# Kernel optimization log

Hardware: AMD Instinct MI355X
Metric: run time of the kernel (lower is better)

The kernel has to match this reference:

```python
import jax, jax.numpy as jnp
import numpy as np

H = 1024          # hidden_dim
N_AVAIL = 32768   # number of available ops (rows of the score matrix)
N_M = 64          # machines
N_OP = 40000      # unfinished ops
N_JOB = 2000      # jobs
L = 4             # policy_num_layers


def setup_inputs() -> dict:
    key = jax.random.key(0)
    ks = jax.random.split(key, 12)
    s_in = (2.0 / (2 * H + 2)) ** 0.5   # kaiming-ish scale
    s_h = (2.0 / H) ** 0.5
    return {
        "x_m": jax.random.normal(ks[0], (N_M, H), jnp.float32),
        "x_op": jax.random.normal(ks[1], (N_OP, H), jnp.float32),
        "job_srpt": jax.random.uniform(ks[2], (N_JOB,), jnp.float32),
        "pt": jax.random.uniform(ks[3], (N_AVAIL,), jnp.float32),  # process_time / max_process_time
        "W0": jax.random.normal(ks[4], (2 * H + 2, H), jnp.float32) * s_in,
        "b0": jnp.zeros((H,), jnp.float32),
        "W1": jax.random.normal(ks[5], (H, H), jnp.float32) * s_h,
        "b1": jnp.zeros((H,), jnp.float32),
        "W2": jax.random.normal(ks[6], (H, H), jnp.float32) * s_h,
        "b2": jnp.zeros((H,), jnp.float32),
        "W3": jax.random.normal(ks[7], (H, 1), jnp.float32) * s_h,
        "b3": jnp.zeros((1,), jnp.float32),
        "m_ids": jax.random.randint(ks[8], (N_AVAIL,), 0, N_M, jnp.int32),
        "op_idx": jax.random.randint(ks[9], (N_AVAIL,), 0, N_OP, jnp.int32),
        "job_ids": jax.random.randint(ks[10], (N_AVAIL,), 0, N_JOB, jnp.int32),
    }


def reference(x_m, x_op, job_srpt, pt, W0, b0, W1, b1, W2, b2, W3, b3,
              m_ids, op_idx, job_ids):
    # Batched gather + concat: replaces the per-op Python loop of torch.cat's.
    feat = jnp.concatenate(
        [x_m[m_ids],                     # [N, H]
         x_op[op_idx],                   # [N, H]
         job_srpt[job_ids][:, None],     # [N, 1]
         pt[:, None]],                   # [N, 1]
        axis=1)                          # [N, 2H+2]
    lrelu = lambda v: jax.nn.leaky_relu(v, 0.01)
    h = lrelu(feat @ W0 + b0)
    h = lrelu(h @ W1 + b1)
    h = lrelu(h @ W2 + b2)
    score = (h @ W3 + b3).ravel()        # [N]
    probs = jax.nn.softmax(score)        # softmax over available ops (dim=0)
    idx = jnp.argmax(score)              # greedy action
    return probs, idx
```

## Files before the change

kernel.cpp:

```cpp
#include <hip/hip_runtime.h>
#include <hip/hip_bf16.h>

typedef __attribute__((ext_vector_type(8))) short short8;
typedef __attribute__((ext_vector_type(4))) float f32x4;

#define GL2LDS16(g, l)                                                         \
  __builtin_amdgcn_global_load_lds(                                            \
      (const __attribute__((address_space(1))) unsigned int*)(g),              \
      (__attribute__((address_space(3))) unsigned int*)(l), 16, 0, 0)

__global__ __launch_bounds__(256) void feat_kernel(
    const float* __restrict__ x_m, const float* __restrict__ x_op,
    const float* __restrict__ job_srpt, const int* __restrict__ m_ids,
    const int* __restrict__ op_idx, const int* __restrict__ job_ids,
    __hip_bfloat16* __restrict__ feat, float* __restrict__ srow) {
  const int row = blockIdx.x;
  const int t = threadIdx.x;
  const int j0 = t * 8;
  const float* src;
  if (j0 < 1024)
    src = x_m + (long)m_ids[row] * 1024 + j0;
  else
    src = x_op + (long)op_idx[row] * 1024 + (j0 - 1024);
  float4 v0 = *(const float4*)src;
  float4 v1 = *(const float4*)(src + 4);
  union {
    __hip_bfloat16 h[8];
    int4 i4;
  } u;
  u.h[0] = __float2bfloat16(v0.x);
  u.h[1] = __float2bfloat16(v0.y);
  u.h[2] = __float2bfloat16(v0.z);
  u.h[3] = __float2bfloat16(v0.w);
  u.h[4] = __float2bfloat16(v1.x);
  u.h[5] = __float2bfloat16(v1.y);
  u.h[6] = __float2bfloat16(v1.z);
  u.h[7] = __float2bfloat16(v1.w);
  *(int4*)&feat[(long)row * 2048 + j0] = u.i4;
  if (t == 0) srow[row] = job_srpt[job_ids[row]];
}

__global__ __launch_bounds__(256) void wconv_kernel(
    const float* __restrict__ W, __hip_bfloat16* __restrict__ Wt, int K) {
  __shared__ float tile[64][65];
  const int kb = blockIdx.x * 64;
  const int nb = blockIdx.y * 64;
  const int t = threadIdx.x;
#pragma unroll
  for (int it = 0; it < 16; ++it) {
    int idx = it * 256 + t;
    int kk = idx >> 6, nn = idx & 63;
    tile[kk][nn] = W[(long)(kb + kk) * 1024 + nb + nn];
  }
  __syncthreads();
#pragma unroll
  for (int it = 0; it < 16; ++it) {
    int idx = it * 256 + t;
    int nn = idx >> 6, kk = idx & 63;
    Wt[(long)(nb + nn) * K + kb + kk] = __float2bfloat16(tile[kk][nn]);
  }
}

__global__ __launch_bounds__(512, 2) void gemm_kernel(
    const __hip_bfloat16* __restrict__ A, const __hip_bfloat16* __restrict__ Bt,
    __hip_bfloat16* __restrict__ C, const float* __restrict__ bias, int M,
    int N, int K, int rank2, const float* __restrict__ wr0,
    const float* __restrict__ wr1, const float* __restrict__ srow,
    const float* __restrict__ ptv, int fuseW3,
    const float* __restrict__ W3, float* __restrict__ scoreOut) {
  __shared__ __align__(16) __hip_bfloat16 As[2][256 * 64];
  __shared__ __align__(16) __hip_bfloat16 Bs[2][256 * 64];
  const int t = threadIdx.x;
  const int lane = t & 63;
  const int wid = t >> 6;
  const int wm = wid >> 2;
  const int wn = wid & 3;
  const long arow0 = (long)blockIdx.x * 256;
  const int bcol0 = blockIdx.y * 256;
  const int NT = K >> 6;

  f32x4 acc[8][4] = {};

  auto stage = [&](int buf, int kt) {
#pragma unroll
    for (int it = 0; it < 4; ++it) {
      int cc = it * 512 + t;
      int r = cc >> 3, c8 = (cc & 7) ^ (r & 7);
      GL2LDS16(A + (arow0 + r) * (long)K + kt * 64 + c8 * 8, &As[buf][cc * 8]);
    }
#pragma unroll
    for (int it = 0; it < 4; ++it) {
      int cc = it * 512 + t;
      int r = cc >> 3, c8 = (cc & 7) ^ (r & 7);
      GL2LDS16(Bt + (long)(bcol0 + r) * (long)K + kt * 64 + c8 * 8,
               &Bs[buf][cc * 8]);
    }
  };

  stage(0, 0);

  for (int kt = 0; kt < NT; ++kt) {
    const int cur = kt & 1;
    if (kt + 1 < NT) {
      stage(cur ^ 1, kt + 1);
      asm volatile("s_waitcnt vmcnt(8)" ::: "memory");
    } else {
      asm volatile("s_waitcnt vmcnt(0)" ::: "memory");
    }
    __builtin_amdgcn_s_barrier();
    asm volatile("" ::: "memory");

#pragma unroll
    for (int ks = 0; ks < 2; ++ks) {
      const int ko = (ks * 32 + ((lane >> 4) << 3)) ^ ((lane & 7) << 3);
      short8 af[8], bfr[4];
#pragma unroll
      for (int i = 0; i < 8; ++i)
        af[i] =
            *(const short8*)&As[cur][(wm * 128 + i * 16 + (lane & 15)) * 64 + ko];
#pragma unroll
      for (int j = 0; j < 4; ++j)
        bfr[j] =
            *(const short8*)&Bs[cur][(wn * 64 + j * 16 + (lane & 15)) * 64 + ko];
#pragma unroll
      for (int i = 0; i < 8; ++i)
#pragma unroll
        for (int j = 0; j < 4; ++j)
          acc[i][j] = __builtin_amdgcn_mfma_f32_16x16x32_bf16(af[i], bfr[j],
                                                              acc[i][j], 0, 0, 0);
    }

    asm volatile("s_waitcnt lgkmcnt(0)" ::: "memory");
    __builtin_amdgcn_s_barrier();
    asm volatile("" ::: "memory");
  }

  if (!fuseW3) {
#pragma unroll
    for (int j = 0; j < 4; ++j) {
      const int c = bcol0 + wn * 64 + j * 16 + (lane & 15);
      const float bia = bias[c];
      float wa = 0.f, wb = 0.f;
      if (rank2) {
        wa = wr0[c];
        wb = wr1[c];
      }
#pragma unroll
      for (int i = 0; i < 8; ++i) {
        const long rb = arow0 + wm * 128 + i * 16 + ((lane >> 4) << 2);
#pragma unroll
        for (int g = 0; g < 4; ++g) {
          const long r = rb + g;
          float v = acc[i][j][g] + bia;
          if (rank2) v += srow[r] * wa + ptv[r] * wb;
          v = v > 0.f ? v : 0.01f * v;
          C[r * N + c] = __float2bfloat16(v);
        }
      }
    }
  } else {
    float bia[4], w3v[4];
#pragma unroll
    for (int j = 0; j < 4; ++j) {
      const int c = bcol0 + wn * 64 + j * 16 + (lane & 15);
      bia[j] = bias[c];
      w3v[j] = W3[c];
    }
#pragma unroll
    for (int i = 0; i < 8; ++i) {
#pragma unroll
      for (int g = 0; g < 4; ++g) {
        float ps = 0.f;
#pragma unroll
        for (int j = 0; j < 4; ++j) {
          float v = acc[i][j][g] + bia[j];
          v = v > 0.f ? v : 0.01f * v;
          ps += v * w3v[j];
        }
        ps += __shfl_xor(ps, 1);
        ps += __shfl_xor(ps, 2);
        ps += __shfl_xor(ps, 4);
        ps += __shfl_xor(ps, 8);
        if ((lane & 15) == 0) {
          const long r = arow0 + wm * 128 + i * 16 + ((lane >> 4) << 2) + g;
          atomicAdd(&scoreOut[r], ps);
        }
      }
    }
  }
}

__global__ __launch_bounds__(256) void redmax_kernel(
    const float* __restrict__ score, float* __restrict__ pmax,
    int* __restrict__ pidx) {
  const int t = threadIdx.x, b = blockIdx.x;
  float m = -1e30f;
  int mi = 0;
#pragma unroll
  for (int u = 0; u < 2; ++u) {
    int i = b * 512 + u * 256 + t;
    float v = score[i];
    if (v > m) {
      m = v;
      mi = i;
    }
  }
  __shared__ float sm[4];
  __shared__ int si[4];
#pragma unroll
  for (int off = 32; off; off >>= 1) {
    float om = __shfl_down(m, off);
    int oi = __shfl_down(mi, off);
    if (om > m || (om == m && oi < mi)) {
      m = om;
      mi = oi;
    }
  }
  const int lane = t & 63, w = t >> 6;
  if (lane == 0) {
    sm[w] = m;
    si[w] = mi;
  }
  __syncthreads();
  if (t == 0) {
    for (int w2 = 1; w2 < 4; ++w2)
      if (sm[w2] > m || (sm[w2] == m && si[w2] < mi)) {
        m = sm[w2];
        mi = si[w2];
      }
    pmax[b] = m;
    pidx[b] = mi;
  }
}

__global__ __launch_bounds__(64) void finmax_kernel(
    const float* __restrict__ pmax, const int* __restrict__ pidx,
    float* __restrict__ gscal, float* __restrict__ out_idx) {
  const int t = threadIdx.x;
  float m = pmax[t];
  int mi = pidx[t];
#pragma unroll
  for (int off = 32; off; off >>= 1) {
    float om = __shfl_down(m, off);
    int oi = __shfl_down(mi, off);
    if (om > m || (om == m && oi < mi)) {
      m = om;
      mi = oi;
    }
  }
  if (t == 0) {
    gscal[0] = m;
    out_idx[0] = (float)mi;
  }
}

__global__ __launch_bounds__(256) void expsum_kernel(
    const float* __restrict__ score, const float* __restrict__ gscal,
    float* __restrict__ e, float* __restrict__ psum) {
  const int t = threadIdx.x, b = blockIdx.x;
  const float gmax = gscal[0];
  float s = 0.f;
#pragma unroll
  for (int u = 0; u < 2; ++u) {
    int i = b * 512 + u * 256 + t;
    float v = expf(score[i] - gmax);
    e[i] = v;
    s += v;
  }
#pragma unroll
  for (int off = 32; off; off >>= 1) s += __shfl_down(s, off);
  __shared__ float sm[4];
  const int lane = t & 63, w = t >> 6;
  if (lane == 0) sm[w] = s;
  __syncthreads();
  if (t == 0) psum[b] = sm[0] + sm[1] + sm[2] + sm[3];
}

__global__ __launch_bounds__(64) void finsum_kernel(const float* __restrict__ psum,
                                                    float* __restrict__ gscal) {
  float s = psum[threadIdx.x];
#pragma unroll
  for (int off = 32; off; off >>= 1) s += __shfl_down(s, off);
  if (threadIdx.x == 0) gscal[1] = 1.0f / s;
}

__global__ __launch_bounds__(256) void scale_kernel(float* __restrict__ e,
                                                    const float* __restrict__ gscal) {
  const float inv = gscal[1];
  const int i = blockIdx.x * 512 + threadIdx.x;
  e[i] *= inv;
  e[i + 256] *= inv;
}

extern "C" void kernel_launch(void* const* d_in, const int* in_sizes, int n_in,
                              void* d_out, int out_size, void* d_ws,
                              size_t ws_size, hipStream_t stream) {
  const float* x_m = (const float*)d_in[0];
  const float* x_op = (const float*)d_in[1];
  const float* job_srpt = (const float*)d_in[2];
  const float* pt = (const float*)d_in[3];
  const float* W0 = (const float*)d_in[4];
  const float* b0 = (const float*)d_in[5];
  const float* W1 = (const float*)d_in[6];
  const float* b1 = (const float*)d_in[7];
  const float* W2 = (const float*)d_in[8];
  const float* b2 = (const float*)d_in[9];
  const float* W3 = (const float*)d_in[10];
  const int* m_ids = (const int*)d_in[12];
  const int* op_idx = (const int*)d_in[13];
  const int* job_ids = (const int*)d_in[14];

  const int M = 32768;

  char* p = (char*)d_ws;
  __hip_bfloat16* feat = (__hip_bfloat16*)p;            p += (size_t)M * 2048 * 2;
  __hip_bfloat16* hA = (__hip_bfloat16*)p;              p += (size_t)M * 1024 * 2;
  __hip_bfloat16* hB = (__hip_bfloat16*)p;              p += (size_t)M * 1024 * 2;
  __hip_bfloat16* Wt0 = (__hip_bfloat16*)p;             p += (size_t)1024 * 2048 * 2;
  __hip_bfloat16* Wt1 = (__hip_bfloat16*)p;             p += (size_t)1024 * 1024 * 2;
  __hip_bfloat16* Wt2 = (__hip_bfloat16*)p;             p += (size_t)1024 * 1024 * 2;
  float* srow = (float*)p;                              p += (size_t)M * 4;
  float* score = (float*)p;                             p += (size_t)M * 4;
  float* pmax = (float*)p;                              p += 256;
  int* pidx = (int*)p;                                  p += 256;
  float* psum = (float*)p;                              p += 256;
  float* gscal = (float*)p;                             p += 256;

  float* probs = (float*)d_out;
  float* out_idx = probs + M;

  feat_kernel<<<M, 256, 0, stream>>>(x_m, x_op, job_srpt, m_ids, op_idx,
                                     job_ids, feat, srow);
  wconv_kernel<<<dim3(32, 16), 256, 0, stream>>>(W0, Wt0, 2048);
  wconv_kernel<<<dim3(16, 16), 256, 0, stream>>>(W1, Wt1, 1024);
  wconv_kernel<<<dim3(16, 16), 256, 0, stream>>>(W2, Wt2, 1024);
  hipMemsetAsync(score, 0, (size_t)M * 4, stream);

  gemm_kernel<<<dim3(128, 4), 512, 0, stream>>>(
      feat, Wt0, hA, b0, M, 1024, 2048, 1, W0 + (size_t)2048 * 1024,
      W0 + (size_t)2049 * 1024, srow, pt, 0, nullptr, nullptr);
  gemm_kernel<<<dim3(128, 4), 512, 0, stream>>>(hA, Wt1, hB, b1, M, 1024, 1024,
                                                0, nullptr, nullptr, nullptr,
                                                nullptr, 0, nullptr, nullptr);
  gemm_kernel<<<dim3(128, 4), 512, 0, stream>>>(hB, Wt2, nullptr, b2, M, 1024,
                                                1024, 0, nullptr, nullptr,
                                                nullptr, nullptr, 1, W3, score);

  redmax_kernel<<<64, 256, 0, stream>>>(score, pmax, pidx);
  finmax_kernel<<<1, 64, 0, stream>>>(pmax, pidx, gscal, out_idx);
  expsum_kernel<<<64, 256, 0, stream>>>(score, gscal, probs, psum);
  finsum_kernel<<<1, 64, 0, stream>>>(psum, gscal);
  scale_kernel<<<64, 256, 0, stream>>>(probs, gscal);
}
```

Before: 457.0 us.

## Split GEMM K-tile into four phases interleaving prefetch with MFMA

The GEMM main loop is restructured so each 64-wide K tile runs in four phases. Each phase issues a quarter of the next tile's global-to-LDS loads, waits only for the A rows it needs, loads those fragments and runs their MFMAs. B fragments are now loaded once per tile and kept in registers. MFMA sections are raised in priority with s_setprio. The aim is to overlap memory traffic with compute more evenly and spread out LDS reads, at the cost of more barriers per tile and more register pressure.

```diff
diff --git a/kernel.cpp b/kernel.cpp
--- a/kernel.cpp
+++ b/kernel.cpp
@@ -79,60 +79,74 @@
   const int bcol0 = blockIdx.y * 256;
   const int NT = K >> 6;
 
+  const int sa_row = ((t >> 8) * 128) + ((t >> 3) & 31);
+  const int sb_row = t >> 3;
+  const int scol = ((t & 7) ^ ((t >> 3) & 7)) * 8;
+
+#define STAGE_A(buf, kt1, p)                                                   \
+  GL2LDS16(A + (arow0 + sa_row + (p) * 32) * (long)K + (kt1) * 64 + scol,      \
+           &As[buf][(t >> 8) * 8192 + (p) * 2048 + (t & 255) * 8])
+#define STAGE_B(buf, kt1, q)                                                   \
+  GL2LDS16(Bt + (long)(bcol0 + sb_row + (q) * 64) * (long)K + (kt1) * 64 + scol, \
+           &Bs[buf][(q) * 4096 + t * 8])
+
   f32x4 acc[8][4] = {};
-
-  auto stage = [&](int buf, int kt) {
-#pragma unroll
-    for (int it = 0; it < 4; ++it) {
-      int cc = it * 512 + t;
-      int r = cc >> 3, c8 = (cc & 7) ^ (r & 7);
-      GL2LDS16(A + (arow0 + r) * (long)K + kt * 64 + c8 * 8, &As[buf][cc * 8]);
-    }
-#pragma unroll
-    for (int it = 0; it < 4; ++it) {
-      int cc = it * 512 + t;
-      int r = cc >> 3, c8 = (cc & 7) ^ (r & 7);
-      GL2LDS16(Bt + (long)(bcol0 + r) * (long)K + kt * 64 + c8 * 8,
-               &Bs[buf][cc * 8]);
-    }
-  };
-
-  stage(0, 0);
+  short8 bfr[8];
+
+#pragma unroll
+  for (int q = 0; q < 4; ++q) STAGE_B(0, 0, q);
+#pragma unroll
+  for (int p = 0; p < 4; ++p) STAGE_A(0, 0, p);
 
   for (int kt = 0; kt < NT; ++kt) {
     const int cur = kt & 1;
-    if (kt + 1 < NT) {
-      stage(cur ^ 1, kt + 1);
-      asm volatile("s_waitcnt vmcnt(8)" ::: "memory");
-    } else {
-      asm volatile("s_waitcnt vmcnt(0)" ::: "memory");
-    }
-    __builtin_amdgcn_s_barrier();
-    asm volatile("" ::: "memory");
-
-#pragma unroll
-    for (int ks = 0; ks < 2; ++ks) {
-      const int ko = (ks * 32 + ((lane >> 4) << 3)) ^ ((lane & 7) << 3);
-      short8 af[8], bfr[4];
-#pragma unroll
-      for (int i = 0; i < 8; ++i)
-        af[i] =
-            *(const short8*)&As[cur][(wm * 128 + i * 16 + (lane & 15)) * 64 + ko];
-#pragma unroll
-      for (int j = 0; j < 4; ++j)
-        bfr[j] =
-            *(const short8*)&Bs[cur][(wn * 64 + j * 16 + (lane & 15)) * 64 + ko];
-#pragma unroll
-      for (int i = 0; i < 8; ++i)
+    const bool pre = (kt + 1) < NT;
+#pragma unroll
+    for (int p = 0; p < 4; ++p) {
+      if (pre) {
+        if (p == 0) { STAGE_B(cur ^ 1, kt + 1, 0); STAGE_B(cur ^ 1, kt + 1, 1); }
+        if (p == 1) { STAGE_B(cur ^ 1, kt + 1, 2); STAGE_B(cur ^ 1, kt + 1, 3); }
+        if (p == 2) { STAGE_A(cur ^ 1, kt + 1, 0); STAGE_A(cur ^ 1, kt + 1, 1); }
+        if (p == 3) { STAGE_A(cur ^ 1, kt + 1, 2); STAGE_A(cur ^ 1, kt + 1, 3); }
+        asm volatile("s_waitcnt vmcnt(4)" ::: "memory");
+      } else {
+        asm volatile("s_waitcnt vmcnt(0)" ::: "memory");
+      }
+      __builtin_amdgcn_s_barrier();
+
+      short8 af[2][2];
+      if (p == 0) {
 #pragma unroll
         for (int j = 0; j < 4; ++j)
-          acc[i][j] = __builtin_amdgcn_mfma_f32_16x16x32_bf16(af[i], bfr[j],
-                                                              acc[i][j], 0, 0, 0);
-    }
-
-    asm volatile("s_waitcnt lgkmcnt(0)" ::: "memory");
-    __builtin_amdgcn_s_barrier();
-    asm volatile("" ::: "memory");
+#pragma unroll
+          for (int ks = 0; ks < 2; ++ks) {
+            const int ko = (ks * 32 + ((lane >> 4) << 3)) ^ ((lane & 7) << 3);
+            bfr[j * 2 + ks] = *(const short8*)
+                &Bs[cur][(wn * 64 + j * 16 + (lane & 15)) * 64 + ko];
+          }
+      }
+#pragma unroll
+      for (int ii = 0; ii < 2; ++ii)
+#pragma unroll
+        for (int ks = 0; ks < 2; ++ks) {
+          const int ko = (ks * 32 + ((lane >> 4) << 3)) ^ ((lane & 7) << 3);
+          af[ii][ks] = *(const short8*)
+              &As[cur][(wm * 128 + (2 * p + ii) * 16 + (lane & 15)) * 64 + ko];
+        }
+
+      asm volatile("s_waitcnt lgkmcnt(0)" ::: "memory");
+      __builtin_amdgcn_s_setprio(1);
+#pragma unroll
+      for (int ii = 0; ii < 2; ++ii)
+#pragma unroll
+        for (int ks = 0; ks < 2; ++ks)
+#pragma unroll
+          for (int j = 0; j < 4; ++j)
+            acc[2 * p + ii][j] = __builtin_amdgcn_mfma_f32_16x16x32_bf16(
+                af[ii][ks], bfr[j * 2 + ks], acc[2 * p + ii][j], 0, 0, 0);
+      __builtin_amdgcn_s_setprio(0);
+      __builtin_amdgcn_s_barrier();
+    }
   }
 
   if (!fuseW3) {
@@ -188,6 +202,8 @@
       }
     }
   }
+#undef STAGE_A
+#undef STAGE_B
 }
 
 __global__ __launch_bounds__(256) void redmax_kernel(
```

Result: faster. 440.0 us (-3.7%).
